# Performance work log

Hardware: AMD Instinct MI355X
Metric: run time of the kernel (lower is better)

## Reference

```python
import jax, jax.numpy as jnp
import numpy as np

T, D, H, E, K = 4096, 1024, 2048, 8, 2  # tokens, model dim, expert hidden, n_experts, top_k
AUX_COEF = 0.01


def setup_inputs() -> dict:
    key = jax.random.key(0)
    ks = jax.random.split(key, 8)
    sd = lambda fan_in: 1.0 / np.sqrt(fan_in)
    x = jax.random.normal(ks[0], (T, D), jnp.float32)
    Wr = jax.random.normal(ks[1], (E, D), jnp.float32) * sd(D)      # router (no bias)
    w1 = jax.random.normal(ks[2], (E, H, D), jnp.float32) * sd(D)   # stacked up-proj
    w2 = jax.random.normal(ks[3], (E, D, H), jnp.float32) * sd(H)   # stacked down-proj
    w3 = jax.random.normal(ks[4], (E, H, D), jnp.float32) * sd(D)   # stacked gate-proj
    w1s = jax.random.normal(ks[5], (H, D), jnp.float32) * sd(D)     # shared expert
    w2s = jax.random.normal(ks[6], (D, H), jnp.float32) * sd(H)
    w3s = jax.random.normal(ks[7], (H, D), jnp.float32) * sd(D)
    return dict(x=x, Wr=Wr, w1=w1, w2=w2, w3=w3, w1s=w1s, w2s=w2s, w3s=w3s)


def _gelu(v):
    return jax.nn.gelu(v, approximate=False)  # torch F.gelu default = exact erf


def reference(x, Wr, w1, w2, w3, w1s, w2s, w3s):
    n_tok = x.shape[0]
    router_out = x @ Wr.T                                   # [T, E]
    router_probs = jax.nn.softmax(router_out, axis=-1)
    _, topk_idx = jax.lax.top_k(router_out, K)              # [T, K]
    topk_probs, _ = jax.lax.top_k(router_probs, K)          # top-k of probs (same order)

    # auxiliary load-balance loss (first-choice density * mean prob)
    expert_mask = jax.nn.one_hot(topk_idx[:, 0], E, dtype=jnp.float32)
    density = expert_mask.mean(axis=0)
    aux_loss = AUX_COEF * jnp.sum(density * router_probs.mean(axis=0)) * E

    # combine weights C[t, e] = sum of routed probs for expert e at token t
    C = jnp.zeros((n_tok, E), x.dtype).at[
        jnp.arange(n_tok)[:, None], topk_idx
    ].add(topk_probs)

    # dense per-expert SwiGLU-style FFN, combined by C (equal math to
    # sort-based dispatch + scatter_add in the original)
    h = _gelu(jnp.einsum('td,ehd->teh', x, w1)) * jnp.einsum('td,ehd->teh', x, w3)
    ye = jnp.einsum('teh,edh->ted', h, w2)                  # [T, E, D]
    out = jnp.einsum('ted,te->td', ye, C)

    # shared expert (always active)
    out = out + (_gelu(x @ w1s.T) * (x @ w3s.T)) @ w2s.T
    return out, aux_loss
```

## Files before the change

kernel.cpp:

```cpp
#include <hip/hip_runtime.h>
#include <hip/hip_bf16.h>
#include <cstdint>

#define T_TOK 4096
#define DMODEL 1024
#define HDIM 2048

typedef short bf16x8 __attribute__((ext_vector_type(8)));
typedef float f32x4 __attribute__((ext_vector_type(4)));
typedef uint32_t u32x4 __attribute__((ext_vector_type(4)));

#define WAITVM(N) asm volatile("s_waitcnt vmcnt(" #N ")" ::: "memory")
#define BARX() asm volatile("s_barrier" ::: "memory")

__device__ __forceinline__ uint32_t cvt_pk_bf16(float lo, float hi) {
  uint32_t d;
  asm("v_cvt_pk_bf16_f32 %0, %1, %2" : "=v"(d) : "v"(lo), "v"(hi));
  return d;
}
__device__ __forceinline__ unsigned short f2bf(float f) {
  uint32_t d;
  asm("v_cvt_pk_bf16_f32 %0, %1, %1" : "=v"(d) : "v"(f));
  return (unsigned short)d;
}
__device__ __forceinline__ float bf2f(unsigned short u) {
  return __uint_as_float((uint32_t)u << 16);
}
__device__ __forceinline__ float gelu_fast(float v) {
  float z = v * 0.70710678118654752f;
  float az = fabsf(z);
  float t = __frcp_rn(1.0f + 0.3275911f * az);
  float poly = ((((1.061405429f * t - 1.453152027f) * t + 1.421413741f) * t
                 - 0.284496736f) * t + 0.254829592f) * t;
  float er = 1.0f - poly * __expf(-z * z);
  er = (z < 0.f) ? -er : er;
  return 0.5f * v * (1.0f + er);
}
__device__ __forceinline__ void gload16(const void* g, void* lds) {
  __builtin_amdgcn_global_load_lds((const __attribute__((address_space(1))) void*)g,
                                   (__attribute__((address_space(3))) void*)lds, 16, 0, 0);
}
__device__ __forceinline__ u32x4 pk8(const float* s) {
  float4 v0 = ((const float4*)s)[0], v1 = ((const float4*)s)[1];
  u32x4 p = {cvt_pk_bf16(v0.x, v0.y), cvt_pk_bf16(v0.z, v0.w),
             cvt_pk_bf16(v1.x, v1.y), cvt_pk_bf16(v1.z, v1.w)};
  return p;
}
__device__ __forceinline__ int xcd_remap(int d, int nblk) {
  int q = nblk >> 3, r = nblk & 7, xc = d & 7, i = d >> 3;
  return (xc < r ? xc * (q + 1) : r * (q + 1) + (xc - r) * q) + i;
}

__global__ __launch_bounds__(256) void prep_kernel(
    const float* __restrict__ x, const float* __restrict__ Wr,
    const float* __restrict__ w1, const float* __restrict__ w3,
    const float* __restrict__ w1s, const float* __restrict__ w3s,
    const float* __restrict__ w2, const float* __restrict__ w2s,
    short* __restrict__ wB, short* __restrict__ wd,
    int* __restrict__ cursor, int* __restrict__ cnt1,
    float* __restrict__ psum, int* __restrict__ perm,
    int* __restrict__ tokpos, float* __restrict__ wtok,
    short* __restrict__ xb) {
  __shared__ float4 sW[8 * 256];
  __shared__ float sP[8];
  int bid = blockIdx.x;
  int tid = threadIdx.x;

  if (bid >= 1024) {
    int cbid = bid - 1024;
    if (cbid < 18432) {
      int id = cbid * 256 + tid;
      int e = id >> 19, rem = id & 524287;
      int nf = rem >> 11, k32 = (rem >> 6) & 31, ln = rem & 63;
      int h = (nf >> 1) * 16 + (ln & 15);
      size_t so = (size_t)h * DMODEL + k32 * 32 + (ln >> 4) * 8;
      const float* src = (nf & 1)
          ? ((e < 8) ? w3 + (size_t)e * 2097152 + so : w3s + so)
          : ((e < 8) ? w1 + (size_t)e * 2097152 + so : w1s + so);
      *(u32x4*)(wB + (size_t)id * 8) = pk8(src);
    } else {
      int id = (cbid - 18432) * 256 + tid;
      int e = id >> 18, rem = id & 262143;
      int d16 = rem >> 12, h32 = (rem >> 6) & 63, ln = rem & 63;
      size_t so = (size_t)(d16 * 16 + (ln & 15)) * HDIM + h32 * 32 + (ln >> 4) * 8;
      const float* s2 = (e < 8) ? w2 + (size_t)e * 2097152 + so : w2s + so;
      *(u32x4*)(wd + (size_t)id * 8) = pk8(s2);
    }
    return;
  }

  const float4* W4 = (const float4*)Wr;
  for (int i = tid; i < 2048; i += 256) sW[i] = W4[i];
  if (tid < 8) sP[tid] = 0.f;
  __syncthreads();

  int lane = tid & 63, wid = tid >> 6;
  int t = bid * 4 + wid;
  float acc[8] = {0.f, 0.f, 0.f, 0.f, 0.f, 0.f, 0.f, 0.f};
  const float4* x4 = (const float4*)(x + (size_t)t * DMODEL);
#pragma unroll
  for (int it = 0; it < 4; ++it) {
    float4 xv = x4[it * 64 + lane];
    uint2 pk = {cvt_pk_bf16(xv.x, xv.y), cvt_pk_bf16(xv.z, xv.w)};
    *(uint2*)(xb + (size_t)t * DMODEL + it * 256 + lane * 4) = pk;
#pragma unroll
    for (int e = 0; e < 8; ++e) {
      float4 wv = sW[e * 256 + it * 64 + lane];
      acc[e] += xv.x * wv.x + xv.y * wv.y + xv.z * wv.z + xv.w * wv.w;
    }
  }
#pragma unroll
  for (int e = 0; e < 8; ++e)
    for (int off = 32; off; off >>= 1) acc[e] += __shfl_xor(acc[e], off);

  float mx = acc[0];
#pragma unroll
  for (int e = 1; e < 8; ++e) mx = fmaxf(mx, acc[e]);
  float ex[8], s = 0.f;
#pragma unroll
  for (int e = 0; e < 8; ++e) { ex[e] = expf(acc[e] - mx); s += ex[e]; }
  float inv = 1.f / s;
  int e0 = 0;
#pragma unroll
  for (int e = 1; e < 8; ++e) if (acc[e] > acc[e0]) e0 = e;
  int e1 = (e0 == 0) ? 1 : 0;
#pragma unroll
  for (int e = 0; e < 8; ++e) if (e != e0 && acc[e] > acc[e1]) e1 = e;

  if (lane == 0) {
#pragma unroll
    for (int e = 0; e < 8; ++e) atomicAdd(&sP[e], ex[e] * inv);
    atomicAdd(&cnt1[e0], 1);
    int s0 = atomicAdd(&cursor[e0], 1);
    perm[e0 * 4096 + s0] = t;
    int s1 = atomicAdd(&cursor[e1], 1);
    perm[e1 * 4096 + s1] = t;
    tokpos[2 * t] = (e0 << 12) | s0;
    tokpos[2 * t + 1] = (e1 << 12) | s1;
    wtok[2 * t] = ex[e0] * inv;
    wtok[2 * t + 1] = ex[e1] * inv;
  }
  __syncthreads();
  if (tid < 8) atomicAdd(&psum[tid], sP[tid]);
}

__global__ void finalize_kernel(const int* __restrict__ cursor,
                                const int* __restrict__ cnt1,
                                const float* __restrict__ psum,
                                int* __restrict__ base,
                                int* __restrict__ work128, int* __restrict__ n128,
                                int* __restrict__ work256, int* __restrict__ n256,
                                float* __restrict__ aux_out) {
  if (threadIdx.x == 0) {
    int b = 0, a1 = 0, a2 = 0;
    for (int e = 0; e < 9; ++e) {
      int c = (e < 8) ? cursor[e] : 4096;
      base[e] = b;
      int t1 = (c + 127) >> 7;
      for (int mt = 0; mt < t1; ++mt) work128[a1++] = (e << 8) | mt;
      int t2 = (c + 255) >> 8;
      for (int mt = 0; mt < t2; ++mt) work256[a2++] = (e << 8) | mt;
      b += t2 << 8;
    }
    *n128 = a1; *n256 = a2;
    float aux = 0.f;
    for (int e = 0; e < 8; ++e)
      aux += ((float)cnt1[e] * (1.f / T_TOK)) * (psum[e] * (1.f / T_TOK));
    aux_out[0] = 0.01f * 8.f * aux;
  }
}

__global__ __launch_bounds__(256, 4) void gemm_upgate(
    const short* __restrict__ xb, const short* __restrict__ wB,
    const int* __restrict__ cursor, const int* __restrict__ base,
    const int* __restrict__ work, const int* __restrict__ nwork,
    const int* __restrict__ perm, unsigned short* __restrict__ hbuf) {
  int nblk = *nwork * 32;
  int d = blockIdx.x;
  if (d >= nblk) return;
  int o = xcd_remap(d, nblk);
  int y = o >> 5, nt = o & 31;
  int wk = work[y];
  int e = wk >> 8, mt = wk & 255;
  int cnt = (e < 8) ? cursor[e] : 4096;
  int hb = base[e];
  const short* wE = wB + (size_t)e * 4194304;

  __shared__ short lds[16384];

  int tid = threadIdx.x, lane = tid & 63, wid = tid >> 6;
  int fr = lane & 15, q4r = lane >> 4;
  int wm = wid >> 1, wn = wid & 1;

  size_t aOff[2], bOff[2];
#pragma unroll
  for (int c = 0; c < 2; ++c) {
    int g = c * 4 + wid;
    int slot = mt * 128 + g * 16 + fr;
    int tok = (e == 8) ? slot : ((slot < cnt) ? perm[e * 4096 + slot] : 0);
    aOff[c] = (size_t)tok * DMODEL + q4r * 8;
    bOff[c] = (size_t)(nt * 8 + g) * 32 * 512 + lane * 8;
  }

  auto stage = [&](int b, int t) {
#pragma unroll
    for (int c = 0; c < 2; ++c) {
      int g = c * 4 + wid;
      gload16(xb + aOff[c] + t * 32, &lds[b * 8192 + g * 512 + lane * 8]);
      gload16(wE + bOff[c] + (size_t)t * 512,
              &lds[b * 8192 + 4096 + g * 512 + lane * 8]);
    }
  };

  f32x4 acc[4][4] = {};

  auto compute = [&](int b) {
    bf16x8 af[4], bf[4];
#pragma unroll
    for (int m = 0; m < 4; ++m)
      af[m] = *(const bf16x8*)&lds[b * 8192 + (wm * 4 + m) * 512 + lane * 8];
#pragma unroll
    for (int n = 0; n < 4; ++n)
      bf[n] = *(const bf16x8*)&lds[b * 8192 + 4096 + (wn * 4 + n) * 512 + lane * 8];
    __builtin_amdgcn_s_setprio(1);
#pragma unroll
    for (int m = 0; m < 4; ++m)
#pragma unroll
      for (int n = 0; n < 4; ++n)
        acc[m][n] = __builtin_amdgcn_mfma_f32_16x16x32_bf16(af[m], bf[n], acc[m][n], 0, 0, 0);
    __builtin_amdgcn_s_setprio(0);
  };

  stage(0, 0);
  __syncthreads();
  int b = 0;
#pragma unroll 1
  for (int t = 0; t < 32; ++t) {
    if (t < 31) stage(b ^ 1, t + 1);
    compute(b);
    __syncthreads();
    b ^= 1;
  }

#pragma unroll
  for (int m = 0; m < 4; ++m) {
#pragma unroll
    for (int p = 0; p < 2; ++p) {
      f32x4 u = acc[m][2 * p], g = acc[m][2 * p + 1];
      int hcol = (nt * 4 + wn * 2 + p) * 16 + fr;
#pragma unroll
      for (int j = 0; j < 4; ++j) {
        int sl = mt * 128 + wm * 64 + m * 16 + q4r * 4 + j;
        float hv = (sl < cnt) ? gelu_fast(u[j]) * g[j] : 0.f;
        hbuf[(size_t)(hb + sl) * HDIM + hcol] = f2bf(hv);
      }
    }
  }
}

__global__ __launch_bounds__(512) void gemm_down8(
    const unsigned short* __restrict__ hbuf, const short* __restrict__ wd,
    const int* __restrict__ base,
    const int* __restrict__ work, const int* __restrict__ nwork,
    unsigned short* __restrict__ yb) {
  int y = blockIdx.y;
  if (y >= *nwork) return;
  int wk = work[y];
  int e = wk >> 8, mt = wk & 255, nt = blockIdx.x;
  int hb = base[e];
  const short* wdE = wd + (size_t)e * 2097152;

  __shared__ short lds[65536];

  int tid = threadIdx.x, lane = tid & 63, wid = tid >> 6;
  int wm = wid >> 2, wn = wid & 3;
  int fr = lane & 15, q4r = lane >> 4;

  size_t aOff[2];
#pragma unroll
  for (int c = 0; c < 2; ++c)
    aOff[c] = (size_t)(hb + mt * 256 + (c * 8 + wid) * 16 + fr) * HDIM + q4r * 8;
  size_t bOff[2];
#pragma unroll
  for (int c = 0; c < 2; ++c)
    bOff[c] = ((size_t)(nt * 16 + c * 8 + wid) * 64) * 512 + lane * 8;

#define DWN_STAGE_A(tt, k32)                                                   \
  { int bb_ = ((tt) & 1) * 32768;                                              \
    gload16(hbuf + aOff[0] + (tt) * 64 + (k32) * 32,                           \
            &lds[bb_ + ((k32) * 16 + wid) * 512 + lane * 8]);                  \
    gload16(hbuf + aOff[1] + (tt) * 64 + (k32) * 32,                           \
            &lds[bb_ + ((k32) * 16 + 8 + wid) * 512 + lane * 8]); }
#define DWN_STAGE_B(tt, k32)                                                   \
  { int bb_ = ((tt) & 1) * 32768;                                              \
    gload16(wdE + bOff[0] + (size_t)((tt) * 2 + (k32)) * 512,                  \
            &lds[bb_ + 16384 + ((k32) * 16 + wid) * 512 + lane * 8]);          \
    gload16(wdE + bOff[1] + (size_t)((tt) * 2 + (k32)) * 512,                  \
            &lds[bb_ + 16384 + ((k32) * 16 + 8 + wid) * 512 + lane * 8]); }
#define DWN_READA(k32, mh)                                                     \
  { _Pragma("unroll") for (int i = 0; i < 4; ++i)                              \
      af[i] = *(const bf16x8*)&lds[bb + ((k32) * 16 + wm * 8 + (mh) * 4 + i) * \
                                       512 + lane * 8]; }
#define DWN_READB(k32)                                                         \
  { _Pragma("unroll") for (int n = 0; n < 4; ++n)                              \
      bf[n] = *(const bf16x8*)&lds[bb + 16384 + ((k32) * 16 + wn * 4 + n) *    \
                                       512 + lane * 8]; }
#define DWN_MFMA(mh)                                                           \
  { __builtin_amdgcn_s_setprio(1);                                             \
    _Pragma("unroll") for (int i = 0; i < 4; ++i)                              \
      _Pragma("unroll") for (int n = 0; n < 4; ++n)                            \
        acc[(mh) * 4 + i][n] = __builtin_amdgcn_mfma_f32_16x16x32_bf16(        \
            af[i], bf[n], acc[(mh) * 4 + i][n], 0, 0, 0);                      \
    __builtin_amdgcn_s_setprio(0); }

  f32x4 acc[8][4] = {};
  bf16x8 af[4], bf[4];

  DWN_STAGE_A(0, 0); DWN_STAGE_B(0, 0); DWN_STAGE_A(0, 1); DWN_STAGE_B(0, 1);
  WAITVM(4); BARX();

#pragma unroll 1
  for (int t = 0; t < 31; ++t) {
    const int bb = (t & 1) * 32768;
    DWN_READA(0, 0); DWN_READB(0); DWN_STAGE_A(t + 1, 0);
    BARX(); DWN_MFMA(0); BARX();
    DWN_READA(0, 1); DWN_STAGE_B(t + 1, 0);
    BARX(); DWN_MFMA(1); WAITVM(4); BARX();
    DWN_READA(1, 0); DWN_READB(1); DWN_STAGE_A(t + 1, 1);
    BARX(); DWN_MFMA(0); BARX();
    DWN_READA(1, 1); DWN_STAGE_B(t + 1, 1);
    BARX(); DWN_MFMA(1); WAITVM(4); BARX();
  }
  {
    const int bb = 32768;
    DWN_READA(0, 0); DWN_READB(0); BARX(); DWN_MFMA(0); BARX();
    DWN_READA(0, 1); BARX(); DWN_MFMA(1); WAITVM(0); BARX();
    DWN_READA(1, 0); DWN_READB(1); BARX(); DWN_MFMA(0); BARX();
    DWN_READA(1, 1); DWN_MFMA(1);
  }

#pragma unroll
  for (int m = 0; m < 8; ++m) {
#pragma unroll
    for (int n = 0; n < 4; ++n) {
      int col = (nt * 16 + wn * 4 + n) * 16 + fr;
      f32x4 a = acc[m][n];
#pragma unroll
      for (int j = 0; j < 4; ++j) {
        int row = mt * 256 + wm * 128 + m * 16 + q4r * 4 + j;
        yb[(size_t)(hb + row) * DMODEL + col] = f2bf(a[j]);
      }
    }
  }
}

__global__ __launch_bounds__(256) void gather_kernel(
    const unsigned short* __restrict__ yb, const int* __restrict__ tokpos,
    const float* __restrict__ wtok, const int* __restrict__ base,
    float* __restrict__ out) {
  int t = blockIdx.x, c4 = threadIdx.x;
  int p0 = tokpos[2 * t], p1 = tokpos[2 * t + 1];
  float w0 = wtok[2 * t], w1 = wtok[2 * t + 1];
  size_t r0 = (size_t)(base[p0 >> 12] + (p0 & 4095)) * DMODEL;
  size_t r1 = (size_t)(base[p1 >> 12] + (p1 & 4095)) * DMODEL;
  size_t rs = (size_t)(base[8] + t) * DMODEL;
  ushort4 v0 = *(const ushort4*)(yb + r0 + c4 * 4);
  ushort4 v1 = *(const ushort4*)(yb + r1 + c4 * 4);
  ushort4 vs = *(const ushort4*)(yb + rs + c4 * 4);
  float4 o;
  o.x = w0 * bf2f(v0.x) + w1 * bf2f(v1.x) + bf2f(vs.x);
  o.y = w0 * bf2f(v0.y) + w1 * bf2f(v1.y) + bf2f(vs.y);
  o.z = w0 * bf2f(v0.z) + w1 * bf2f(v1.z) + bf2f(vs.z);
  o.w = w0 * bf2f(v0.w) + w1 * bf2f(v1.w) + bf2f(vs.w);
  *(float4*)(out + (size_t)t * DMODEL + c4 * 4) = o;
}

extern "C" void kernel_launch(void* const* d_in, const int* in_sizes, int n_in,
                              void* d_out, int out_size, void* d_ws, size_t ws_size,
                              hipStream_t stream) {
  const float* x   = (const float*)d_in[0];
  const float* Wr  = (const float*)d_in[1];
  const float* w1  = (const float*)d_in[2];
  const float* w2  = (const float*)d_in[3];
  const float* w3  = (const float*)d_in[4];
  const float* w1s = (const float*)d_in[5];
  const float* w2s = (const float*)d_in[6];
  const float* w3s = (const float*)d_in[7];
  float* out = (float*)d_out;

  char* ws = (char*)d_ws;
  const size_t HBUF_OFF = 0;
  const size_t XB_OFF   = 58720256;
  const size_t WB_OFF   = XB_OFF + 8388608;
  const size_t WD_OFF   = WB_OFF + 75497472;
  const size_t PERM_OFF = WD_OFF + 37748736;
  const size_t TP_OFF   = PERM_OFF + 131072;
  const size_t WT_OFF   = TP_OFF + 32768;
  const size_t CTRL_OFF = WT_OFF + 32768;
  const size_t W128_OFF = CTRL_OFF + 256;
  const size_t W256_OFF = W128_OFF + 512;

  unsigned short* hbuf = (unsigned short*)(ws + HBUF_OFF);
  short* xb = (short*)(ws + XB_OFF);
  short* wB = (short*)(ws + WB_OFF);
  short* wd = (short*)(ws + WD_OFF);
  unsigned short* yb = (unsigned short*)(ws + WB_OFF);
  int*   perm   = (int*)(ws + PERM_OFF);
  int*   tokpos = (int*)(ws + TP_OFF);
  float* wtok   = (float*)(ws + WT_OFF);
  int*   cursor = (int*)(ws + CTRL_OFF);
  int*   cnt1   = (int*)(ws + CTRL_OFF + 64);
  float* psum   = (float*)(ws + CTRL_OFF + 128);
  int*   base   = (int*)(ws + CTRL_OFF + 192);
  int*   n128   = (int*)(ws + CTRL_OFF + 236);
  int*   n256   = (int*)(ws + CTRL_OFF + 240);
  int*   work128 = (int*)(ws + W128_OFF);
  int*   work256 = (int*)(ws + W256_OFF);

  hipMemsetAsync(ws + CTRL_OFF, 0, 256, stream);

  prep_kernel<<<28672, 256, 0, stream>>>(x, Wr, w1, w3, w1s, w3s, w2, w2s,
                                         wB, wd, cursor, cnt1, psum, perm,
                                         tokpos, wtok, xb);
  finalize_kernel<<<1, 64, 0, stream>>>(cursor, cnt1, psum, base,
                                        work128, n128, work256, n256,
                                        out + (size_t)T_TOK * DMODEL);
  gemm_upgate<<<3328, 256, 0, stream>>>(xb, wB, cursor, base, work128, n128,
                                        perm, hbuf);
  gemm_down8<<<dim3(4, 64), 512, 0, stream>>>(hbuf, wd, base, work256, n256, yb);
  gather_kernel<<<4096, 256, 0, stream>>>(yb, tokpos, wtok, base, out);
}
```

Baseline: 381.4 us.

## Move w2 bf16 conversion into up/gate GEMM launch and drop router LDS staging

The down-projection weight conversion (w2/w2s to bf16 tiled layout) moves out of the prep kernel and into extra trailing blocks of the up/gate GEMM launch. Those conversion blocks can then overlap with the GEMM's tail instead of lengthening prep. Block indices in prep are reordered so weight-conversion blocks come first and router blocks last. The router weights are now read straight from global memory instead of being staged in LDS. This shortens the prep critical path, at the cost of GEMM blocks competing with memory-bound conversion work and more global/L2 reads of Wr.

```diff
diff --git a/kernel.cpp b/kernel.cpp
--- a/kernel.cpp
+++ b/kernel.cpp
@@ -51,53 +51,39 @@
   return (xc < r ? xc * (q + 1) : r * (q + 1) + (xc - r) * q) + i;
 }
 
-__global__ __launch_bounds__(256) void prep_kernel(
+__global__ __launch_bounds__(256) void prep1_kernel(
     const float* __restrict__ x, const float* __restrict__ Wr,
     const float* __restrict__ w1, const float* __restrict__ w3,
     const float* __restrict__ w1s, const float* __restrict__ w3s,
-    const float* __restrict__ w2, const float* __restrict__ w2s,
-    short* __restrict__ wB, short* __restrict__ wd,
+    short* __restrict__ wB,
     int* __restrict__ cursor, int* __restrict__ cnt1,
     float* __restrict__ psum, int* __restrict__ perm,
     int* __restrict__ tokpos, float* __restrict__ wtok,
     short* __restrict__ xb) {
-  __shared__ float4 sW[8 * 256];
   __shared__ float sP[8];
-  int bid = blockIdx.x;
-  int tid = threadIdx.x;
-
-  if (bid >= 1024) {
-    int cbid = bid - 1024;
-    if (cbid < 18432) {
-      int id = cbid * 256 + tid;
-      int e = id >> 19, rem = id & 524287;
-      int nf = rem >> 11, k32 = (rem >> 6) & 31, ln = rem & 63;
-      int h = (nf >> 1) * 16 + (ln & 15);
-      size_t so = (size_t)h * DMODEL + k32 * 32 + (ln >> 4) * 8;
-      const float* src = (nf & 1)
-          ? ((e < 8) ? w3 + (size_t)e * 2097152 + so : w3s + so)
-          : ((e < 8) ? w1 + (size_t)e * 2097152 + so : w1s + so);
-      *(u32x4*)(wB + (size_t)id * 8) = pk8(src);
-    } else {
-      int id = (cbid - 18432) * 256 + tid;
-      int e = id >> 18, rem = id & 262143;
-      int d16 = rem >> 12, h32 = (rem >> 6) & 63, ln = rem & 63;
-      size_t so = (size_t)(d16 * 16 + (ln & 15)) * HDIM + h32 * 32 + (ln >> 4) * 8;
-      const float* s2 = (e < 8) ? w2 + (size_t)e * 2097152 + so : w2s + so;
-      *(u32x4*)(wd + (size_t)id * 8) = pk8(s2);
-    }
+  int bid = blockIdx.x, tid = threadIdx.x;
+
+  if (bid < 18432) {
+    int id = bid * 256 + tid;
+    int e = id >> 19, rem = id & 524287;
+    int nf = rem >> 11, k32 = (rem >> 6) & 31, ln = rem & 63;
+    int h = (nf >> 1) * 16 + (ln & 15);
+    size_t so = (size_t)h * DMODEL + k32 * 32 + (ln >> 4) * 8;
+    const float* src = (nf & 1)
+        ? ((e < 8) ? w3 + (size_t)e * 2097152 + so : w3s + so)
+        : ((e < 8) ? w1 + (size_t)e * 2097152 + so : w1s + so);
+    *(u32x4*)(wB + (size_t)id * 8) = pk8(src);
     return;
   }
 
-  const float4* W4 = (const float4*)Wr;
-  for (int i = tid; i < 2048; i += 256) sW[i] = W4[i];
   if (tid < 8) sP[tid] = 0.f;
   __syncthreads();
 
   int lane = tid & 63, wid = tid >> 6;
-  int t = bid * 4 + wid;
+  int t = (bid - 18432) * 4 + wid;
   float acc[8] = {0.f, 0.f, 0.f, 0.f, 0.f, 0.f, 0.f, 0.f};
   const float4* x4 = (const float4*)(x + (size_t)t * DMODEL);
+  const float4* W4 = (const float4*)Wr;
 #pragma unroll
   for (int it = 0; it < 4; ++it) {
     float4 xv = x4[it * 64 + lane];
@@ -105,7 +91,7 @@
     *(uint2*)(xb + (size_t)t * DMODEL + it * 256 + lane * 4) = pk;
 #pragma unroll
     for (int e = 0; e < 8; ++e) {
-      float4 wv = sW[e * 256 + it * 64 + lane];
+      float4 wv = W4[e * 256 + it * 64 + lane];
       acc[e] += xv.x * wv.x + xv.y * wv.y + xv.z * wv.z + xv.w * wv.w;
     }
   }
@@ -170,11 +156,25 @@
   }
 }
 
-__global__ __launch_bounds__(256, 4) void gemm_upgate(
+__global__ __launch_bounds__(256, 4) void gemm_upgate_f(
     const short* __restrict__ xb, const short* __restrict__ wB,
+    const float* __restrict__ w2, const float* __restrict__ w2s,
+    short* __restrict__ wd,
     const int* __restrict__ cursor, const int* __restrict__ base,
     const int* __restrict__ work, const int* __restrict__ nwork,
     const int* __restrict__ perm, unsigned short* __restrict__ hbuf) {
+  __shared__ short lds[16384];
+
+  if (blockIdx.x >= 3328) {
+    int id = (blockIdx.x - 3328) * 256 + threadIdx.x;
+    int e = id >> 18, rem = id & 262143;
+    int d16 = rem >> 12, h32 = (rem >> 6) & 63, ln = rem & 63;
+    size_t so = (size_t)(d16 * 16 + (ln & 15)) * HDIM + h32 * 32 + (ln >> 4) * 8;
+    const float* s2 = (e < 8) ? w2 + (size_t)e * 2097152 + so : w2s + so;
+    *(u32x4*)(wd + (size_t)id * 8) = pk8(s2);
+    return;
+  }
+
   int nblk = *nwork * 32;
   int d = blockIdx.x;
   if (d >= nblk) return;
@@ -185,8 +185,6 @@
   int cnt = (e < 8) ? cursor[e] : 4096;
   int hb = base[e];
   const short* wE = wB + (size_t)e * 4194304;
-
-  __shared__ short lds[16384];
 
   int tid = threadIdx.x, lane = tid & 63, wid = tid >> 6;
   int fr = lane & 15, q4r = lane >> 4;
@@ -419,14 +417,15 @@
 
   hipMemsetAsync(ws + CTRL_OFF, 0, 256, stream);
 
-  prep_kernel<<<28672, 256, 0, stream>>>(x, Wr, w1, w3, w1s, w3s, w2, w2s,
-                                         wB, wd, cursor, cnt1, psum, perm,
-                                         tokpos, wtok, xb);
+  prep1_kernel<<<19456, 256, 0, stream>>>(x, Wr, w1, w3, w1s, w3s, wB,
+                                          cursor, cnt1, psum, perm,
+                                          tokpos, wtok, xb);
   finalize_kernel<<<1, 64, 0, stream>>>(cursor, cnt1, psum, base,
                                         work128, n128, work256, n256,
                                         out + (size_t)T_TOK * DMODEL);
-  gemm_upgate<<<3328, 256, 0, stream>>>(xb, wB, cursor, base, work128, n128,
-                                        perm, hbuf);
+  gemm_upgate_f<<<12544, 256, 0, stream>>>(xb, wB, w2, w2s, wd,
+                                           cursor, base, work128, n128,
+                                           perm, hbuf);
   gemm_down8<<<dim3(4, 64), 512, 0, stream>>>(hbuf, wd, base, work256, n256, yb);
   gather_kernel<<<4096, 256, 0, stream>>>(yb, tokpos, wtok, base, out);
 }
```

New measurement: 372.2 us. 2.4% less time.
